# Kernel tuning notes

Hardware: AMD Instinct MI355X
Metric: run time of the kernel (lower is better)

The kernel has to match this reference:

```python
import jax, jax.numpy as jnp
import numpy as np

# Static configuration (matches init_kwargs / input_specs)
NUM_SEQS = 8          # sequences in the batch
H = 32                # query heads
H_KV = 8              # kv heads (GQA group = 4)
D = 128               # head dim
MEM_BLK = 64          # paged-cache block size (tokens per cache block)
CTX = 2048            # cached context length per sequence (uniform)
Q = 64                # new (diffusion-block) tokens per sequence
MAX_BLKS = CTX // MEM_BLK   # 32 blocks per sequence in block_tables
N_BLOCKS = 512        # total cache blocks in the pool
SCALE = 1.0 / float(np.sqrt(D))


def setup_inputs() -> dict:
    key = jax.random.key(0)
    k0, k1, k2, k3, k4 = jax.random.split(key, 5)
    T = NUM_SEQS * Q  # total new tokens (flat ragged layout)
    q = jax.random.normal(k0, (T, H, D), dtype=jnp.float32)
    k = jax.random.normal(k1, (T, H_KV, D), dtype=jnp.float32)
    v = jax.random.normal(k2, (T, H_KV, D), dtype=jnp.float32)
    k_cache = jax.random.normal(k3, (N_BLOCKS, MEM_BLK, H_KV, D), dtype=jnp.float32)
    v_cache = jax.random.normal(k4, (N_BLOCKS, MEM_BLK, H_KV, D), dtype=jnp.float32)
    # sequence s owns cache blocks [s*MAX_BLKS, (s+1)*MAX_BLKS)
    block_tables = jnp.arange(NUM_SEQS * MAX_BLKS, dtype=jnp.int32).reshape(NUM_SEQS, MAX_BLKS)
    # new tokens are written into freshly allocated slots beyond the context blocks
    slot_mapping = NUM_SEQS * MAX_BLKS * MEM_BLK + jnp.arange(T, dtype=jnp.int32)
    return {"q": q, "k": k, "v": v, "k_cache": k_cache, "v_cache": v_cache,
            "block_tables": block_tables, "slot_mapping": slot_mapping}


def reference(q, k, v, k_cache, v_cache, block_tables, slot_mapping):
    # --- store_kvcache: scatter new k/v rows into flat cache slots ---
    kc_flat = k_cache.reshape(-1, H_KV, D).at[slot_mapping].set(k)
    vc_flat = v_cache.reshape(-1, H_KV, D).at[slot_mapping].set(v)
    kc = kc_flat.reshape(N_BLOCKS, MEM_BLK, H_KV, D)
    vc = vc_flat.reshape(N_BLOCKS, MEM_BLK, H_KV, D)

    # --- load_kvcache: block-table indexed gather of context, concat new kv ---
    # ctx_k/ctx_v: [S, CTX, H_KV, D]
    ctx_k = kc[block_tables].reshape(NUM_SEQS, MAX_BLKS * MEM_BLK, H_KV, D)[:, :CTX]
    ctx_v = vc[block_tables].reshape(NUM_SEQS, MAX_BLKS * MEM_BLK, H_KV, D)[:, :CTX]
    k_new = k.reshape(NUM_SEQS, Q, H_KV, D)
    v_new = v.reshape(NUM_SEQS, Q, H_KV, D)
    k_full = jnp.concatenate([ctx_k, k_new], axis=1)  # [S, CTX+Q, H_KV, D]
    v_full = jnp.concatenate([ctx_v, v_new], axis=1)

    # --- flex attention with GQA: diffusion block attends to full context +
    #     bidirectionally within its own new block ---
    G = H // H_KV
    qg = q.reshape(NUM_SEQS, Q, H_KV, G, D)
    # scores: [S, H_KV, G, Q, CTX+Q]
    scores = jnp.einsum("sqhgd,skhd->shgqk", qg, k_full) * SCALE
    attn = jax.nn.softmax(scores, axis=-1)
    out = jnp.einsum("shgqk,skhd->sqhgd", attn, v_full)  # [S, Q, H_KV, G, D]
    return out.reshape(NUM_SEQS * Q, H, D)
```

## Files before the change

### kernel.cpp

```cpp
#include <hip/hip_runtime.h>
#include <hip/hip_bf16.h>


typedef float  f32x16 __attribute__((ext_vector_type(16)));
typedef short  bf16x8 __attribute__((ext_vector_type(8)));

__device__ __forceinline__ unsigned pkbf(float lo, float hi) {
    union { __hip_bfloat162 h; unsigned u; } t;
    t.h.x = __float2bfloat16(lo);
    t.h.y = __float2bfloat16(hi);
    return t.u;
}
__device__ __forceinline__ float bf2f(unsigned short u) {
    return __uint_as_float((unsigned)u << 16);
}

#define BARRIER_LGKM() asm volatile("s_waitcnt lgkmcnt(0)\n\ts_barrier" ::: "memory")

#define OWS_ELEMS (4u * 64u * 256u * 128u)

__launch_bounds__(512, 2)
__global__ void attn_part(const float* __restrict__ qg,
                          const float* __restrict__ kin,
                          const float* __restrict__ vin,
                          const float* __restrict__ kcache,
                          const float* __restrict__ vcache,
                          const int*   __restrict__ bt,
                          __hip_bfloat16* __restrict__ Ows,
                          float* __restrict__ Lws)
{
    __shared__ __align__(16) unsigned char smem[32768];

    const int bid   = blockIdx.x;
    const int grp   = bid & 63;
    const int slice = bid >> 6;
    const int s     = grp >> 3;
    const int hkv   = grp & 7;

    const int tid  = threadIdx.x;
    const int w    = tid >> 6;
    const int lane = tid & 63;
    const int l32  = lane & 31;
    const int hi2  = lane >> 5;
    const int g    = w >> 1;
    const int qh   = w & 1;

    unsigned char* KB = smem;
    unsigned char* VB = smem + 16384;

    const float QSCALE = 0.08838834764831845f * 1.44269504088896340736f;

    bf16x8 aq[8];
    {
        const float* qp =
            qg + (size_t)((s * 64 + qh * 32 + l32) * 32 + hkv * 4 + g) * 128;
#pragma unroll
        for (int dc = 0; dc < 8; ++dc) {
            const float* p = qp + dc * 16 + hi2 * 8;
            const float4 f0 = *(const float4*)(p);
            const float4 f1 = *(const float4*)(p + 4);
            uint4 tt = make_uint4(pkbf(f0.x * QSCALE, f0.y * QSCALE),
                                  pkbf(f0.z * QSCALE, f0.w * QSCALE),
                                  pkbf(f1.x * QSCALE, f1.y * QSCALE),
                                  pkbf(f1.z * QSCALE, f1.w * QSCALE));
            aq[dc] = __builtin_bit_cast(bf16x8, tt);
        }
    }

    f32x16 acco[4];
#pragma unroll
    for (int dc = 0; dc < 4; ++dc) acco[dc] = (f32x16)0.f;
    float lsum = 0.f;

    const int vd  = tid & 127;
    const int vkg = tid >> 7;

    float4 kreg[2];
    float  vreg[8];

    const int tile0 = (slice < 2) ? slice * 17 : 34 + (slice - 2) * 16;
    const int nt    = (slice < 2) ? 17 : 16;

    auto load_regs = [&](int T) {
        const float *ks, *vs;
        if (T < 64) {
            const int blk = bt[s * 32 + (T >> 1)];
            const size_t base = (size_t)blk * 65536 + (size_t)(T & 1) * 32768 + hkv * 128;
            ks = kcache + base; vs = vcache + base;
        } else {
            const size_t base = (size_t)(s * 64 + (T & 1) * 32) * 1024 + hkv * 128;
            ks = kin + base; vs = vin + base;
        }
#pragma unroll
        for (int i = 0; i < 2; ++i) {
            const int f = tid + 512 * i;
            kreg[i] = *(const float4*)(ks + (size_t)(f >> 5) * 1024 + (f & 31) * 4);
        }
#pragma unroll
        for (int j = 0; j < 8; ++j)
            vreg[j] = vs[(size_t)(vkg * 8 + j) * 1024 + vd];
    };

    auto write_lds = [&](int buf) {
        unsigned char* K = KB + buf * 8192;
        unsigned char* V = VB + buf * 8192;
#pragma unroll
        for (int i = 0; i < 2; ++i) {
            const int f  = tid + 512 * i;
            const int kv = f >> 5;
            const int dk = f & 31;
            const int Xs = dk ^ ((kv & 15) << 1);
            *(uint2*)(K + kv * 256 + Xs * 8) =
                make_uint2(pkbf(kreg[i].x, kreg[i].y), pkbf(kreg[i].z, kreg[i].w));
        }
        const int u = vkg ^ ((vd >> 1) & 3);
        *(uint4*)(V + vd * 64 + u * 16) =
            make_uint4(pkbf(vreg[0], vreg[1]), pkbf(vreg[2], vreg[3]),
                       pkbf(vreg[4], vreg[5]), pkbf(vreg[6], vreg[7]));
    };

    const int vq = (l32 >> 1) & 3;

    auto compute = [&](int buf) {
        const unsigned char* K = KB + buf * 8192;
        const unsigned char* V = VB + buf * 8192;

        f32x16 sc = (f32x16)0.f;
#pragma unroll
        for (int dc = 0; dc < 8; ++dc) {
            const int u = (dc * 2 + hi2) ^ (l32 & 15);
            const bf16x8 ak = *(const bf16x8*)(K + l32 * 256 + u * 16);
            sc = __builtin_amdgcn_mfma_f32_32x32x16_bf16(ak, aq[dc], sc, 0, 0, 0);
        }

        float p[16];
#pragma unroll
        for (int r = 0; r < 16; ++r) {
            p[r] = __builtin_amdgcn_exp2f(sc[r]);
            lsum += p[r];
        }

        unsigned A0 = pkbf(p[0],  p[1]),  A1 = pkbf(p[2],  p[3]);
        unsigned B0 = pkbf(p[4],  p[5]),  B1 = pkbf(p[6],  p[7]);
        unsigned C0 = pkbf(p[8],  p[9]),  C1 = pkbf(p[10], p[11]);
        unsigned D0 = pkbf(p[12], p[13]), D1 = pkbf(p[14], p[15]);
        asm volatile("v_permlane32_swap_b32 %0, %1" : "+v"(A0), "+v"(B0));
        asm volatile("v_permlane32_swap_b32 %0, %1" : "+v"(A1), "+v"(B1));
        asm volatile("v_permlane32_swap_b32 %0, %1" : "+v"(C0), "+v"(D0));
        asm volatile("v_permlane32_swap_b32 %0, %1" : "+v"(C1), "+v"(D1));
        bf16x8 pa[2];
        {
            uint4 t0 = make_uint4(A0, A1, B0, B1);
            uint4 t1 = make_uint4(C0, C1, D0, D1);
            pa[0] = __builtin_bit_cast(bf16x8, t0);
            pa[1] = __builtin_bit_cast(bf16x8, t1);
        }

#pragma unroll
        for (int kk = 0; kk < 2; ++kk)
#pragma unroll
            for (int d2 = 0; d2 < 4; ++d2) {
                const int u = (kk * 2 + hi2) ^ vq;
                const bf16x8 bv = *(const bf16x8*)(V + (d2 * 32 + l32) * 64 + u * 16);
                acco[d2] = __builtin_amdgcn_mfma_f32_32x32x16_bf16(pa[kk], bv, acco[d2], 0, 0, 0);
            }
    };

    load_regs(tile0);
    write_lds(0);
    load_regs(tile0 + 1);

    for (int tt = 0; tt < nt; ++tt) {
        BARRIER_LGKM();
        if (tt + 1 < nt) write_lds((tt + 1) & 1);
        if (tt + 2 < nt) load_regs(tile0 + tt + 2);
        compute(tt & 1);
    }

    const float lt = lsum + __shfl_xor(lsum, 32);
    const size_t gq = (size_t)(slice * 64 + grp) * 256 + w * 32;
    if (hi2 == 0) Lws[gq + l32] = lt;
    __hip_bfloat16* Od = Ows + gq * 128;
#pragma unroll
    for (int dc = 0; dc < 4; ++dc)
#pragma unroll
        for (int r = 0; r < 16; ++r) {
            const int qiw = (r & 3) + 8 * (r >> 2) + 4 * hi2;
            Od[(size_t)qiw * 128 + dc * 32 + l32] = __float2bfloat16(acco[dc][r]);
        }
}

__launch_bounds__(256)
__global__ void attn_combine(const __hip_bfloat16* __restrict__ Ows,
                             const float* __restrict__ Lws,
                             float* __restrict__ out)
{
    const int idx = blockIdx.x * 256 + threadIdx.x;
    const int dq  = idx & 31;
    const int qr  = (idx >> 5) & 255;
    const int grp = idx >> 13;
    const int s = grp >> 3, hkv = grp & 7;
    const int g = qr >> 6, qtok = qr & 63;

    float4 acc = make_float4(0.f, 0.f, 0.f, 0.f);
    float  l   = 0.f;
#pragma unroll
    for (int sl = 0; sl < 4; ++sl) {
        const size_t base = (size_t)(sl * 64 + grp) * 256 + qr;
        const ushort4 p = *(const ushort4*)(Ows + base * 128 + dq * 4);
        acc.x += bf2f(p.x); acc.y += bf2f(p.y);
        acc.z += bf2f(p.z); acc.w += bf2f(p.w);
        l += Lws[base];
    }
    const float inv = 1.0f / l;
    float4 o = make_float4(acc.x * inv, acc.y * inv, acc.z * inv, acc.w * inv);
    *(float4*)(out + ((size_t)((s * 64 + qtok) * 32 + hkv * 4 + g)) * 128 + dq * 4) = o;
}

extern "C" void kernel_launch(void* const* d_in, const int* in_sizes, int n_in,
                              void* d_out, int out_size, void* d_ws, size_t ws_size,
                              hipStream_t stream)
{
    const float* q  = (const float*)d_in[0];
    const float* k  = (const float*)d_in[1];
    const float* v  = (const float*)d_in[2];
    const float* kc = (const float*)d_in[3];
    const float* vc = (const float*)d_in[4];
    const int*   bt = (const int*)d_in[5];
    __hip_bfloat16* Ows = (__hip_bfloat16*)d_ws;
    float* Lws = (float*)((char*)d_ws + (size_t)OWS_ELEMS * 2);
    float* o   = (float*)d_out;

    attn_part<<<dim3(256), dim3(512), 0, stream>>>(q, k, v, kc, vc, bt, Ows, Lws);
    attn_combine<<<dim3(2048), dim3(256), 0, stream>>>(Ows, Lws, o);
}
```

Before: 42.25 us.

## Double pipeline tile size to 64 keys per stage with larger LDS buffers

Each pipeline stage now loads and stages 64 keys (one full cache block) instead of 32, doubling the LDS buffers to 64KB and the register staging arrays. Half as many barriers are needed, and each barrier interval holds two compute sub-steps, which amortizes synchronization and gives the loads more time to land. Occupancy hint drops from 2 to 1 block per CU, and the tile split across slices changes to 9/8/8/8 tiles. The trade is higher register and LDS pressure and lower occupancy in exchange for fewer sync points.

```diff
diff --git a/kernel.cpp b/kernel.cpp
--- a/kernel.cpp
+++ b/kernel.cpp
@@ -19,7 +19,7 @@
 
 #define OWS_ELEMS (4u * 64u * 256u * 128u)
 
-__launch_bounds__(512, 2)
+__launch_bounds__(512, 1)
 __global__ void attn_part(const float* __restrict__ qg,
                           const float* __restrict__ kin,
                           const float* __restrict__ vin,
@@ -29,7 +29,7 @@
                           __hip_bfloat16* __restrict__ Ows,
                           float* __restrict__ Lws)
 {
-    __shared__ __align__(16) unsigned char smem[32768];
+    __shared__ __align__(16) unsigned char smem[65536];
 
     const int bid   = blockIdx.x;
     const int grp   = bid & 63;
@@ -46,7 +46,7 @@
     const int qh   = w & 1;
 
     unsigned char* KB = smem;
-    unsigned char* VB = smem + 16384;
+    unsigned char* VB = smem + 32768;
 
     const float QSCALE = 0.08838834764831845f * 1.44269504088896340736f;
 
@@ -75,55 +75,65 @@
     const int vd  = tid & 127;
     const int vkg = tid >> 7;
 
-    float4 kreg[2];
-    float  vreg[8];
-
-    const int tile0 = (slice < 2) ? slice * 17 : 34 + (slice - 2) * 16;
-    const int nt    = (slice < 2) ? 17 : 16;
+    float4 kreg[4];
+    float  vreg[16];
+
+    const int tile0 = slice * 8 + (slice > 0 ? 1 : 0);
+    const int nt    = 8 + (slice == 0 ? 1 : 0);
 
     auto load_regs = [&](int T) {
         const float *ks, *vs;
-        if (T < 64) {
-            const int blk = bt[s * 32 + (T >> 1)];
-            const size_t base = (size_t)blk * 65536 + (size_t)(T & 1) * 32768 + hkv * 128;
+        if (T < 32) {
+            const int blk = bt[s * 32 + T];
+            const size_t base = (size_t)blk * 65536 + hkv * 128;
             ks = kcache + base; vs = vcache + base;
         } else {
-            const size_t base = (size_t)(s * 64 + (T & 1) * 32) * 1024 + hkv * 128;
+            const size_t base = (size_t)(s * 64) * 1024 + hkv * 128;
             ks = kin + base; vs = vin + base;
         }
 #pragma unroll
-        for (int i = 0; i < 2; ++i) {
+        for (int i = 0; i < 4; ++i) {
             const int f = tid + 512 * i;
             kreg[i] = *(const float4*)(ks + (size_t)(f >> 5) * 1024 + (f & 31) * 4);
         }
 #pragma unroll
-        for (int j = 0; j < 8; ++j)
-            vreg[j] = vs[(size_t)(vkg * 8 + j) * 1024 + vd];
+        for (int sub = 0; sub < 2; ++sub)
+#pragma unroll
+            for (int j = 0; j < 8; ++j)
+                vreg[sub * 8 + j] =
+                    vs[(size_t)(sub * 32 + vkg * 8 + j) * 1024 + vd];
     };
 
     auto write_lds = [&](int buf) {
-        unsigned char* K = KB + buf * 8192;
-        unsigned char* V = VB + buf * 8192;
-#pragma unroll
-        for (int i = 0; i < 2; ++i) {
-            const int f  = tid + 512 * i;
-            const int kv = f >> 5;
-            const int dk = f & 31;
-            const int Xs = dk ^ ((kv & 15) << 1);
-            *(uint2*)(K + kv * 256 + Xs * 8) =
+#pragma unroll
+        for (int i = 0; i < 4; ++i) {
+            const int f   = tid + 512 * i;
+            const int kv  = f >> 5;
+            const int sub = kv >> 5;
+            const int kvs = kv & 31;
+            const int dk  = f & 31;
+            const int Xs  = dk ^ ((kvs & 15) << 1);
+            unsigned char* K = KB + buf * 16384 + sub * 8192;
+            *(uint2*)(K + kvs * 256 + Xs * 8) =
                 make_uint2(pkbf(kreg[i].x, kreg[i].y), pkbf(kreg[i].z, kreg[i].w));
         }
         const int u = vkg ^ ((vd >> 1) & 3);
-        *(uint4*)(V + vd * 64 + u * 16) =
-            make_uint4(pkbf(vreg[0], vreg[1]), pkbf(vreg[2], vreg[3]),
-                       pkbf(vreg[4], vreg[5]), pkbf(vreg[6], vreg[7]));
+#pragma unroll
+        for (int sub = 0; sub < 2; ++sub) {
+            unsigned char* V = VB + buf * 16384 + sub * 8192;
+            *(uint4*)(V + vd * 64 + u * 16) =
+                make_uint4(pkbf(vreg[sub * 8 + 0], vreg[sub * 8 + 1]),
+                           pkbf(vreg[sub * 8 + 2], vreg[sub * 8 + 3]),
+                           pkbf(vreg[sub * 8 + 4], vreg[sub * 8 + 5]),
+                           pkbf(vreg[sub * 8 + 6], vreg[sub * 8 + 7]));
+        }
     };
 
     const int vq = (l32 >> 1) & 3;
 
-    auto compute = [&](int buf) {
-        const unsigned char* K = KB + buf * 8192;
-        const unsigned char* V = VB + buf * 8192;
+    auto compute = [&](int buf, int sub) {
+        const unsigned char* K = KB + buf * 16384 + sub * 8192;
+        const unsigned char* V = VB + buf * 16384 + sub * 8192;
 
         f32x16 sc = (f32x16)0.f;
 #pragma unroll
@@ -174,7 +184,8 @@
         BARRIER_LGKM();
         if (tt + 1 < nt) write_lds((tt + 1) & 1);
         if (tt + 2 < nt) load_regs(tile0 + tt + 2);
-        compute(tt & 1);
+        compute(tt & 1, 0);
+        compute(tt & 1, 1);
     }
 
     const float lt = lsum + __shfl_xor(lsum, 32);
```

Result: slower. 43.94 us (+4.0%).

## Deepen global-to-LDS prefetch to two register sets with unrolled loop

Applied to the files above, without the earlier changes.

Adds a second register staging set so global loads for tile t+3 are issued while tile t is computed, and manually unrolls the main loop by two so the LDS buffer indices are compile-time constants. The aim is to hide more global-memory latency behind MFMA work. Occupancy hint drops from 2 to 1 workgroup per SIMD-group to allow the extra registers, which reduces the latency hiding that comes from running concurrent waves.

```diff
diff --git a/kernel.cpp b/kernel.cpp
--- a/kernel.cpp
+++ b/kernel.cpp
@@ -19,7 +19,7 @@
 
 #define OWS_ELEMS (4u * 64u * 256u * 128u)
 
-__launch_bounds__(512, 2)
+__launch_bounds__(512, 1)
 __global__ void attn_part(const float* __restrict__ qg,
                           const float* __restrict__ kin,
                           const float* __restrict__ vin,
@@ -75,14 +75,13 @@
     const int vd  = tid & 127;
     const int vkg = tid >> 7;
 
-    float4 kreg[2];
-    float  vreg[8];
+    float4 kregA[2], kregB[2];
+    float  vregA[8], vregB[8];
 
     const int tile0 = (slice < 2) ? slice * 17 : 34 + (slice - 2) * 16;
     const int nt    = (slice < 2) ? 17 : 16;
 
-    auto load_regs = [&](int T) {
-        const float *ks, *vs;
+    auto src_for = [&](int T, const float*& ks, const float*& vs) {
         if (T < 64) {
             const int blk = bt[s * 32 + (T >> 1)];
             const size_t base = (size_t)blk * 65536 + (size_t)(T & 1) * 32768 + hkv * 128;
@@ -91,33 +90,43 @@
             const size_t base = (size_t)(s * 64 + (T & 1) * 32) * 1024 + hkv * 128;
             ks = kin + base; vs = vin + base;
         }
-#pragma unroll
-        for (int i = 0; i < 2; ++i) {
-            const int f = tid + 512 * i;
-            kreg[i] = *(const float4*)(ks + (size_t)(f >> 5) * 1024 + (f & 31) * 4);
-        }
-#pragma unroll
-        for (int j = 0; j < 8; ++j)
-            vreg[j] = vs[(size_t)(vkg * 8 + j) * 1024 + vd];
     };
 
-    auto write_lds = [&](int buf) {
-        unsigned char* K = KB + buf * 8192;
-        unsigned char* V = VB + buf * 8192;
-#pragma unroll
-        for (int i = 0; i < 2; ++i) {
-            const int f  = tid + 512 * i;
-            const int kv = f >> 5;
-            const int dk = f & 31;
-            const int Xs = dk ^ ((kv & 15) << 1);
-            *(uint2*)(K + kv * 256 + Xs * 8) =
-                make_uint2(pkbf(kreg[i].x, kreg[i].y), pkbf(kreg[i].z, kreg[i].w));
-        }
-        const int u = vkg ^ ((vd >> 1) & 3);
-        *(uint4*)(V + vd * 64 + u * 16) =
-            make_uint4(pkbf(vreg[0], vreg[1]), pkbf(vreg[2], vreg[3]),
-                       pkbf(vreg[4], vreg[5]), pkbf(vreg[6], vreg[7]));
-    };
+#define LOAD_REGS(SET, T)                                                         \
+    do {                                                                          \
+        const float *ks_, *vs_;                                                   \
+        src_for((T), ks_, vs_);                                                   \
+        _Pragma("unroll")                                                         \
+        for (int i = 0; i < 2; ++i) {                                             \
+            const int f = tid + 512 * i;                                          \
+            kreg##SET[i] = *(const float4*)(ks_ + (size_t)(f >> 5) * 1024 + (f & 31) * 4); \
+        }                                                                         \
+        _Pragma("unroll")                                                         \
+        for (int j = 0; j < 8; ++j)                                               \
+            vreg##SET[j] = vs_[(size_t)(vkg * 8 + j) * 1024 + vd];                \
+    } while (0)
+
+#define WRITE_LDS(SET, BUF)                                                       \
+    do {                                                                          \
+        unsigned char* K_ = KB + (BUF) * 8192;                                    \
+        unsigned char* V_ = VB + (BUF) * 8192;                                    \
+        _Pragma("unroll")                                                         \
+        for (int i = 0; i < 2; ++i) {                                             \
+            const int f  = tid + 512 * i;                                         \
+            const int kv = f >> 5;                                                \
+            const int dk = f & 31;                                                \
+            const int Xs = dk ^ ((kv & 15) << 1);                                 \
+            *(uint2*)(K_ + kv * 256 + Xs * 8) =                                   \
+                make_uint2(pkbf(kreg##SET[i].x, kreg##SET[i].y),                  \
+                           pkbf(kreg##SET[i].z, kreg##SET[i].w));                 \
+        }                                                                         \
+        const int u_ = vkg ^ ((vd >> 1) & 3);                                     \
+        *(uint4*)(V_ + vd * 64 + u_ * 16) =                                       \
+            make_uint4(pkbf(vreg##SET[0], vreg##SET[1]),                          \
+                       pkbf(vreg##SET[2], vreg##SET[3]),                          \
+                       pkbf(vreg##SET[4], vreg##SET[5]),                          \
+                       pkbf(vreg##SET[6], vreg##SET[7]));                         \
+    } while (0)
 
     const int vq = (l32 >> 1) & 3;
 
@@ -166,15 +175,25 @@
             }
     };
 
-    load_regs(tile0);
-    write_lds(0);
-    load_regs(tile0 + 1);
-
-    for (int tt = 0; tt < nt; ++tt) {
+    LOAD_REGS(A, tile0);
+    WRITE_LDS(A, 0);
+    LOAD_REGS(B, tile0 + 1);
+    LOAD_REGS(A, tile0 + 2);
+
+    int tt = 0;
+    while (true) {
         BARRIER_LGKM();
-        if (tt + 1 < nt) write_lds((tt + 1) & 1);
-        if (tt + 2 < nt) load_regs(tile0 + tt + 2);
-        compute(tt & 1);
+        if (tt + 1 < nt) WRITE_LDS(B, 1);
+        if (tt + 3 < nt) LOAD_REGS(B, tile0 + tt + 3);
+        compute(0);
+        if (tt + 1 >= nt) break;
+
+        BARRIER_LGKM();
+        if (tt + 2 < nt) WRITE_LDS(A, 0);
+        if (tt + 4 < nt) LOAD_REGS(A, tile0 + tt + 4);
+        compute(1);
+        tt += 2;
+        if (tt >= nt) break;
     }
 
     const float lt = lsum + __shfl_xor(lsum, 32);
```

Result: no change. 41.64 us (median of 2 runs) (-1.4%).
